# Kernel optimization log

Hardware: AMD Instinct MI355X
Metric: run time of the kernel (lower is better)

## Reference

```python
import jax, jax.numpy as jnp
import numpy as np

TAU = 1.0


def setup_inputs() -> dict:
    key = jax.random.key(0)
    k1, k2, k3 = jax.random.split(key, 3)
    B, S, V = 2, 2048, 32000
    p = jax.random.normal(k1, (B, S, V), dtype=jnp.float32)
    q = jax.random.normal(k2, (B, S, V), dtype=jnp.float32)
    mask = jax.random.randint(k3, (B, S), 0, 2).astype(bool)
    return {"p": p, "q": q, "mask": mask}


def reference(p, q, mask):
    # Faithful to the torch module: p[mask], q[mask] selects valid tokens;
    # here we keep static shapes and weight by the mask instead.
    lp = jax.nn.log_softmax(p / TAU, axis=-1)   # [B,S,V] log-probs
    lq = jax.nn.log_softmax(q / TAU, axis=-1)
    m = 0.5 * (lp + lq)                          # mean of LOG-probs (as in source)
    # KLDivLoss(log_target=True)(input=m, target=lp) = sum exp(lp) * (lp - m)
    kl_p = jnp.sum(jnp.exp(lp) * (lp - m), axis=-1)  # [B,S]
    kl_q = jnp.sum(jnp.exp(lq) * (lq - m), axis=-1)  # [B,S]
    w = mask.astype(lp.dtype)
    n = jnp.maximum(jnp.sum(w), 1.0)  # batchmean: divide by masked-token count
    return 0.5 * jnp.sum((kl_p + kl_q) * w) / n
```

## Files before the change

kernel.cpp:

```cpp
#include <hip/hip_runtime.h>
#include <math.h>

#define THREADS 256
#define LOG2E 1.44269504088896340736f
#define LN2   0.69314718055994530942f

__device__ __forceinline__ void merge3(float& m, float& s, float& t,
                                       float m2, float s2, float t2) {
    float nm = fmaxf(m, m2);
    float c1 = exp2f(m  - nm);
    float c2 = exp2f(m2 - nm);
    s = s * c1 + s2 * c2;
    t = t * c1 + t2 * c2;
    m = nm;
}

__global__ __launch_bounds__(THREADS, 4) void jsd_rows(
    const float* __restrict__ p, const float* __restrict__ q,
    const int* __restrict__ mask, float* __restrict__ rows, int V)
{
    const int row = blockIdx.x;
    if (mask[row] == 0) {
        if (threadIdx.x == 0) rows[row] = 0.0f;
        return;
    }
    const int tid = threadIdx.x;
    const size_t base = (size_t)row * (size_t)V;
    const float4* p4 = reinterpret_cast<const float4*>(p + base);
    const float4* q4 = reinterpret_cast<const float4*>(q + base);
    const int n4 = V >> 2;
    const int n8 = n4 >> 1;

    float mp = -INFINITY, sp = 0.f, tp = 0.f;
    float mq = -INFINITY, sq = 0.f, tq = 0.f;

    for (int i = tid; i < n8; i += THREADS) {
        const float4 a0 = p4[2 * i];
        const float4 a1 = p4[2 * i + 1];
        const float4 b0 = q4[2 * i];
        const float4 b1 = q4[2 * i + 1];

        float ya[8], yb[8], d[8];
        ya[0] = a0.x * LOG2E; ya[1] = a0.y * LOG2E; ya[2] = a0.z * LOG2E; ya[3] = a0.w * LOG2E;
        ya[4] = a1.x * LOG2E; ya[5] = a1.y * LOG2E; ya[6] = a1.z * LOG2E; ya[7] = a1.w * LOG2E;
        yb[0] = b0.x * LOG2E; yb[1] = b0.y * LOG2E; yb[2] = b0.z * LOG2E; yb[3] = b0.w * LOG2E;
        yb[4] = b1.x * LOG2E; yb[5] = b1.y * LOG2E; yb[6] = b1.z * LOG2E; yb[7] = b1.w * LOG2E;
        #pragma unroll
        for (int k = 0; k < 8; ++k) d[k] = ya[k] - yb[k];

        {
            float c01 = fmaxf(ya[0], ya[1]), c23 = fmaxf(ya[2], ya[3]);
            float c45 = fmaxf(ya[4], ya[5]), c67 = fmaxf(ya[6], ya[7]);
            float cm  = fmaxf(fmaxf(c01, c23), fmaxf(c45, c67));
            float nm  = fmaxf(mp, cm);
            float sc  = exp2f(mp - nm);
            float e[8];
            #pragma unroll
            for (int k = 0; k < 8; ++k) e[k] = exp2f(ya[k] - nm);
            float es = ((e[0] + e[1]) + (e[2] + e[3])) + ((e[4] + e[5]) + (e[6] + e[7]));
            float g0 = __builtin_fmaf(e[1], d[1], e[0] * d[0]);
            float g1 = __builtin_fmaf(e[3], d[3], e[2] * d[2]);
            float g2 = __builtin_fmaf(e[5], d[5], e[4] * d[4]);
            float g3 = __builtin_fmaf(e[7], d[7], e[6] * d[6]);
            float ts = (g0 + g1) + (g2 + g3);
            sp = __builtin_fmaf(sp, sc, es);
            tp = __builtin_fmaf(tp, sc, ts);
            mp = nm;
        }
        {
            float c01 = fmaxf(yb[0], yb[1]), c23 = fmaxf(yb[2], yb[3]);
            float c45 = fmaxf(yb[4], yb[5]), c67 = fmaxf(yb[6], yb[7]);
            float cm  = fmaxf(fmaxf(c01, c23), fmaxf(c45, c67));
            float nm  = fmaxf(mq, cm);
            float sc  = exp2f(mq - nm);
            float e[8];
            #pragma unroll
            for (int k = 0; k < 8; ++k) e[k] = exp2f(yb[k] - nm);
            float es = ((e[0] + e[1]) + (e[2] + e[3])) + ((e[4] + e[5]) + (e[6] + e[7]));
            float g0 = __builtin_fmaf(e[1], d[1], e[0] * d[0]);
            float g1 = __builtin_fmaf(e[3], d[3], e[2] * d[2]);
            float g2 = __builtin_fmaf(e[5], d[5], e[4] * d[4]);
            float g3 = __builtin_fmaf(e[7], d[7], e[6] * d[6]);
            float ts = (g0 + g1) + (g2 + g3);
            sq = __builtin_fmaf(sq, sc, es);
            tq = __builtin_fmaf(tq, sc, ts);
            mq = nm;
        }
    }

    if (n4 & 1) {
        int i = n8 * 2;
        if (tid == 0) {
            float4 a = p4[i], b = q4[i];
            float xa[4] = {a.x, a.y, a.z, a.w};
            float xb[4] = {b.x, b.y, b.z, b.w};
            #pragma unroll
            for (int k = 0; k < 4; ++k) {
                float yA = xa[k] * LOG2E, yB = xb[k] * LOG2E, dd = yA - yB;
                float nm = fmaxf(mp, yA), sc = exp2f(mp - nm), e = exp2f(yA - nm);
                sp = sp * sc + e; tp = tp * sc + e * dd; mp = nm;
                nm = fmaxf(mq, yB); sc = exp2f(mq - nm); e = exp2f(yB - nm);
                sq = sq * sc + e; tq = tq * sc + e * dd; mq = nm;
            }
        }
    }

    #pragma unroll
    for (int off = 1; off < 64; off <<= 1) {
        merge3(mp, sp, tp,
               __shfl_xor(mp, off, 64), __shfl_xor(sp, off, 64), __shfl_xor(tp, off, 64));
        merge3(mq, sq, tq,
               __shfl_xor(mq, off, 64), __shfl_xor(sq, off, 64), __shfl_xor(tq, off, 64));
    }

    __shared__ float red[THREADS / 64][6];
    const int wave = tid >> 6;
    const int lane = tid & 63;
    if (lane == 0) {
        red[wave][0] = mp; red[wave][1] = sp; red[wave][2] = tp;
        red[wave][3] = mq; red[wave][4] = sq; red[wave][5] = tq;
    }
    __syncthreads();
    if (tid == 0) {
        float Mp = red[0][0], Sp = red[0][1], Tp = red[0][2];
        float Mq = red[0][3], Sq = red[0][4], Tq = red[0][5];
        #pragma unroll
        for (int w = 1; w < THREADS / 64; ++w) {
            merge3(Mp, Sp, Tp, red[w][0], red[w][1], red[w][2]);
            merge3(Mq, Sq, Tq, red[w][3], red[w][4], red[w][5]);
        }
        rows[row] = LN2 * (Tp / Sp - Tq / Sq);
    }
}

__global__ __launch_bounds__(256) void jsd_final(
    const float* __restrict__ rows, const int* __restrict__ mask,
    float* __restrict__ out, int R)
{
    const int tid = threadIdx.x;
    float sum = 0.f, cnt = 0.f;
    for (int i = tid; i < R; i += 256) {
        sum += rows[i];
        cnt += (mask[i] != 0) ? 1.0f : 0.0f;
    }
    #pragma unroll
    for (int off = 1; off < 64; off <<= 1) {
        sum += __shfl_xor(sum, off, 64);
        cnt += __shfl_xor(cnt, off, 64);
    }
    __shared__ float ssum[4], scnt[4];
    const int wave = tid >> 6;
    const int lane = tid & 63;
    if (lane == 0) { ssum[wave] = sum; scnt[wave] = cnt; }
    __syncthreads();
    if (tid == 0) {
        float S = 0.f, C = 0.f;
        #pragma unroll
        for (int w = 0; w < 4; ++w) { S += ssum[w]; C += scnt[w]; }
        out[0] = 0.25f * S / fmaxf(C, 1.0f);
    }
}

extern "C" void kernel_launch(void* const* d_in, const int* in_sizes, int n_in,
                              void* d_out, int out_size, void* d_ws, size_t ws_size,
                              hipStream_t stream) {
    const float* p    = (const float*)d_in[0];
    const float* q    = (const float*)d_in[1];
    const int*   mask = (const int*)d_in[2];
    float*       out  = (float*)d_out;

    const int BS = in_sizes[2];
    const int V  = in_sizes[0] / BS;

    float* rows = (float*)d_ws;

    jsd_rows<<<BS, THREADS, 0, stream>>>(p, q, mask, rows, V);
    jsd_final<<<1, 256, 0, stream>>>(rows, mask, out, BS);
}
```

Before: 117.0 us.

## Split each row across four blocks and merge online-softmax partials in final kernel

```diff
diff --git a/kernel.cpp b/kernel.cpp
--- a/kernel.cpp
+++ b/kernel.cpp
@@ -2,8 +2,11 @@
 #include <math.h>
 
 #define THREADS 256
+#define PARTS   4
 #define LOG2E 1.44269504088896340736f
 #define LN2   0.69314718055994530942f
+
+typedef float fx4 __attribute__((ext_vector_type(4)));
 
 __device__ __forceinline__ void merge3(float& m, float& s, float& t,
                                        float m2, float s2, float t2) {
@@ -15,36 +18,41 @@
     m = nm;
 }
 
-__global__ __launch_bounds__(THREADS, 4) void jsd_rows(
+__global__ __launch_bounds__(THREADS) void jsd_rows(
     const float* __restrict__ p, const float* __restrict__ q,
-    const int* __restrict__ mask, float* __restrict__ rows, int V)
+    const int* __restrict__ mask, float* __restrict__ partials, int V)
 {
-    const int row = blockIdx.x;
-    if (mask[row] == 0) {
-        if (threadIdx.x == 0) rows[row] = 0.0f;
-        return;
-    }
+    const int row  = blockIdx.x >> 2;
+    const int part = blockIdx.x & (PARTS - 1);
+    if (mask[row] == 0) return;
+
     const int tid = threadIdx.x;
     const size_t base = (size_t)row * (size_t)V;
-    const float4* p4 = reinterpret_cast<const float4*>(p + base);
-    const float4* q4 = reinterpret_cast<const float4*>(q + base);
-    const int n4 = V >> 2;
-    const int n8 = n4 >> 1;
+    const fx4* p4 = reinterpret_cast<const fx4*>(p + base);
+    const fx4* q4 = reinterpret_cast<const fx4*>(q + base);
+
+    const int n8  = V >> 3;
+    const int cpp = (n8 + PARTS - 1) / PARTS;
+    const int c0  = part * cpp;
+    const int c1e = min(c0 + cpp, n8);
 
     float mp = -INFINITY, sp = 0.f, tp = 0.f;
     float mq = -INFINITY, sq = 0.f, tq = 0.f;
 
-    for (int i = tid; i < n8; i += THREADS) {
-        const float4 a0 = p4[2 * i];
-        const float4 a1 = p4[2 * i + 1];
-        const float4 b0 = q4[2 * i];
-        const float4 b1 = q4[2 * i + 1];
+    for (int i = c0 + tid; i < c1e; i += THREADS) {
+        const fx4 a0 = __builtin_nontemporal_load(p4 + 2 * i);
+        const fx4 a1 = __builtin_nontemporal_load(p4 + 2 * i + 1);
+        const fx4 b0 = __builtin_nontemporal_load(q4 + 2 * i);
+        const fx4 b1 = __builtin_nontemporal_load(q4 + 2 * i + 1);
 
         float ya[8], yb[8], d[8];
-        ya[0] = a0.x * LOG2E; ya[1] = a0.y * LOG2E; ya[2] = a0.z * LOG2E; ya[3] = a0.w * LOG2E;
-        ya[4] = a1.x * LOG2E; ya[5] = a1.y * LOG2E; ya[6] = a1.z * LOG2E; ya[7] = a1.w * LOG2E;
-        yb[0] = b0.x * LOG2E; yb[1] = b0.y * LOG2E; yb[2] = b0.z * LOG2E; yb[3] = b0.w * LOG2E;
-        yb[4] = b1.x * LOG2E; yb[5] = b1.y * LOG2E; yb[6] = b1.z * LOG2E; yb[7] = b1.w * LOG2E;
+        #pragma unroll
+        for (int k = 0; k < 4; ++k) {
+            ya[k]     = a0[k] * LOG2E;
+            ya[k + 4] = a1[k] * LOG2E;
+            yb[k]     = b0[k] * LOG2E;
+            yb[k + 4] = b1[k] * LOG2E;
+        }
         #pragma unroll
         for (int k = 0; k < 8; ++k) d[k] = ya[k] - yb[k];
 
@@ -88,20 +96,13 @@
         }
     }
 
-    if (n4 & 1) {
-        int i = n8 * 2;
-        if (tid == 0) {
-            float4 a = p4[i], b = q4[i];
-            float xa[4] = {a.x, a.y, a.z, a.w};
-            float xb[4] = {b.x, b.y, b.z, b.w};
-            #pragma unroll
-            for (int k = 0; k < 4; ++k) {
-                float yA = xa[k] * LOG2E, yB = xb[k] * LOG2E, dd = yA - yB;
-                float nm = fmaxf(mp, yA), sc = exp2f(mp - nm), e = exp2f(yA - nm);
-                sp = sp * sc + e; tp = tp * sc + e * dd; mp = nm;
-                nm = fmaxf(mq, yB); sc = exp2f(mq - nm); e = exp2f(yB - nm);
-                sq = sq * sc + e; tq = tq * sc + e * dd; mq = nm;
-            }
+    if (part == PARTS - 1 && (V & 7) && tid == 0) {
+        for (int j = n8 * 8; j < V; ++j) {
+            float yA = p[base + j] * LOG2E, yB = q[base + j] * LOG2E, dd = yA - yB;
+            float nm = fmaxf(mp, yA), sc = exp2f(mp - nm), e = exp2f(yA - nm);
+            sp = sp * sc + e; tp = tp * sc + e * dd; mp = nm;
+            nm = fmaxf(mq, yB); sc = exp2f(mq - nm); e = exp2f(yB - nm);
+            sq = sq * sc + e; tq = tq * sc + e * dd; mq = nm;
         }
     }
 
@@ -129,26 +130,37 @@
             merge3(Mp, Sp, Tp, red[w][0], red[w][1], red[w][2]);
             merge3(Mq, Sq, Tq, red[w][3], red[w][4], red[w][5]);
         }
-        rows[row] = LN2 * (Tp / Sp - Tq / Sq);
+        float* dst = partials + (size_t)blockIdx.x * 6;
+        dst[0] = Mp; dst[1] = Sp; dst[2] = Tp;
+        dst[3] = Mq; dst[4] = Sq; dst[5] = Tq;
     }
 }
 
-__global__ __launch_bounds__(256) void jsd_final(
-    const float* __restrict__ rows, const int* __restrict__ mask,
+__global__ __launch_bounds__(1024) void jsd_final(
+    const float* __restrict__ partials, const int* __restrict__ mask,
     float* __restrict__ out, int R)
 {
     const int tid = threadIdx.x;
     float sum = 0.f, cnt = 0.f;
-    for (int i = tid; i < R; i += 256) {
-        sum += rows[i];
-        cnt += (mask[i] != 0) ? 1.0f : 0.0f;
+    for (int r = tid; r < R; r += 1024) {
+        if (mask[r] == 0) continue;
+        const float* pr = partials + (size_t)r * PARTS * 6;
+        float Mp = pr[0], Sp = pr[1], Tp = pr[2];
+        float Mq = pr[3], Sq = pr[4], Tq = pr[5];
+        #pragma unroll
+        for (int w = 1; w < PARTS; ++w) {
+            merge3(Mp, Sp, Tp, pr[6*w + 0], pr[6*w + 1], pr[6*w + 2]);
+            merge3(Mq, Sq, Tq, pr[6*w + 3], pr[6*w + 4], pr[6*w + 5]);
+        }
+        sum += LN2 * (Tp / Sp - Tq / Sq);
+        cnt += 1.0f;
     }
     #pragma unroll
     for (int off = 1; off < 64; off <<= 1) {
         sum += __shfl_xor(sum, off, 64);
         cnt += __shfl_xor(cnt, off, 64);
     }
-    __shared__ float ssum[4], scnt[4];
+    __shared__ float ssum[16], scnt[16];
     const int wave = tid >> 6;
     const int lane = tid & 63;
     if (lane == 0) { ssum[wave] = sum; scnt[wave] = cnt; }
@@ -156,7 +168,7 @@
     if (tid == 0) {
         float S = 0.f, C = 0.f;
         #pragma unroll
-        for (int w = 0; w < 4; ++w) { S += ssum[w]; C += scnt[w]; }
+        for (int w = 0; w < 16; ++w) { S += ssum[w]; C += scnt[w]; }
         out[0] = 0.25f * S / fmaxf(C, 1.0f);
     }
 }
@@ -172,8 +184,8 @@
     const int BS = in_sizes[2];
     const int V  = in_sizes[0] / BS;
 
-    float* rows = (float*)d_ws;
+    float* partials = (float*)d_ws;
 
-    jsd_rows<<<BS, THREADS, 0, stream>>>(p, q, mask, rows, V);
-    jsd_final<<<1, 256, 0, stream>>>(rows, mask, out, BS);
+    jsd_rows<<<BS * PARTS, THREADS, 0, stream>>>(p, q, mask, partials, V);
+    jsd_final<<<1, 1024, 0, stream>>>(partials, mask, out, BS);
 }
```

After: 107.6 us. 8.0% less time.
